# Optimization experiments

Measured on AMD Instinct MI355X. Metric: run time of the kernel, lower is better.

Reference implementation:

```python
import jax, jax.numpy as jnp
import numpy as np

NUM_HEADS = 16
INACTIVE = 4          # cfg_comp.attention_heads_inactive
SIG_DIM = 64          # cfg_comp.attention_heads_signature_dim
MLP_HIDDEN = 512      # cfg_comp.attention_heads_inference_mlp_hidden


def setup_inputs() -> dict:
    key = jax.random.key(0)
    ks = jax.random.split(key, 16)
    S, B, E = 2048, 2, 1024
    def xavier(k, shape, gain=1.0):
        fan_in, fan_out = shape[1], shape[0]
        a = gain * np.sqrt(6.0 / (fan_in + fan_out))
        return jax.random.uniform(k, shape, jnp.float32, -a, a)
    g = 1.0 / np.sqrt(2.0)
    return {
        "query": jax.random.normal(ks[0], (S, B, E), jnp.float32),
        "q_w": xavier(ks[1], (E, E), g), "q_b": jnp.zeros((E,), jnp.float32),
        "k_w": xavier(ks[2], (E, E), g), "k_b": jnp.zeros((E,), jnp.float32),
        "v_w": xavier(ks[3], (E, E), g), "v_b": jnp.zeros((E,), jnp.float32),
        "out_w": xavier(ks[4], (E, E)), "out_b": jnp.zeros((E,), jnp.float32),
        "inf1_w": xavier(ks[5], (MLP_HIDDEN, E), np.sqrt(2.0)),
        "inf1_b": jnp.zeros((MLP_HIDDEN,), jnp.float32),
        "inf2_w": xavier(ks[6], (SIG_DIM, MLP_HIDDEN), np.sqrt(2.0)),
        "inf2_b": jnp.zeros((SIG_DIM,), jnp.float32),
        "head_sig": jax.random.normal(ks[7], (NUM_HEADS, SIG_DIM), jnp.float32)
                    * np.sqrt(2.0 / (NUM_HEADS + SIG_DIM)),
    }


def _head_mask(query, inf1_w, inf1_b, inf2_w, inf2_b, head_sig):
    # inference_masking_step: (S, B, E) -> binary mask (B, H, S)
    t = jax.nn.relu(query @ inf1_w.T + inf1_b)          # (S, B, hidden)
    t = t @ inf2_w.T + inf2_b                            # (S, B, sig)
    s = t @ head_sig.T                                   # (S, B, H) head scores
    keep = NUM_HEADS - INACTIVE
    kth = jax.lax.top_k(s, keep)[0][..., -1]             # (S, B) kth-largest score
    mask = (s >= kth[..., None]).astype(query.dtype)     # 1 at top-`keep` heads
    mask = jax.lax.stop_gradient(mask)                   # scatter of constants in torch
    return jnp.transpose(mask, (1, 2, 0))                # (B, H, S)


def reference(query, q_w, q_b, k_w, k_b, v_w, v_b, out_w, out_b,
              inf1_w, inf1_b, inf2_w, inf2_b, head_sig):
    S, B, E = query.shape
    H, D = NUM_HEADS, E // NUM_HEADS
    scaling = D ** (-0.5)

    q = (query @ q_w.T + q_b) * scaling                  # (S, B, E)
    k = query @ k_w.T + k_b
    v = query @ v_w.T + v_b
    # (S, B, E) -> (B, H, S, D)
    to_bhsd = lambda x: jnp.transpose(x.reshape(S, B, H, D), (1, 2, 0, 3))
    q, k, v = to_bhsd(q), to_bhsd(k), to_bhsd(v)

    attn = jax.nn.softmax(jnp.einsum("bhqd,bhkd->bhqk", q, k), axis=-1)
    o = jnp.einsum("bhqk,bhkd->bhqd", attn, v)           # (B, H, S, D)

    mask = _head_mask(query, inf1_w, inf1_b, inf2_w, inf2_b, head_sig)  # (B, H, S)
    o = o * mask[..., None]                              # gate per head per position

    out = jnp.transpose(o, (2, 0, 1, 3)).reshape(S, B, E)
    return out @ out_w.T + out_b
```

## Files before the change

kernel.cpp:

```cpp
#include <hip/hip_runtime.h>
#include <hip/hip_bf16.h>

#define S_LEN 2048
#define BATCH 2
#define EDIM 1024
#define NHEAD 16
#define DHEAD 64
#define HIDDEN 512
#define SIGD 64
#define KEEP 12

typedef __attribute__((ext_vector_type(8))) short bf16x8;
typedef __attribute__((ext_vector_type(4))) float f32x4;

static __device__ __forceinline__ float bf2f(short s) {
  unsigned int u = ((unsigned int)(unsigned short)s) << 16;
  float f; __builtin_memcpy(&f, &u, 4); return f;
}
static __device__ __forceinline__ short f2bf(float f) {
  unsigned int u; __builtin_memcpy(&u, &f, 4);
  u += 0x7fffu + ((u >> 16) & 1u);
  return (short)(u >> 16);
}

static __device__ __forceinline__ void gl_lds16(const short* g, short* l) {
  __builtin_amdgcn_global_load_lds(
      (const __attribute__((address_space(1))) unsigned int*)g,
      (__attribute__((address_space(3))) unsigned int*)l, 16, 0, 0);
}

template<int CTRL>
static __device__ __forceinline__ float dpp_movf(float x) {
  return __builtin_bit_cast(float, __builtin_amdgcn_update_dpp(
      0, __builtin_bit_cast(int, x), CTRL, 0xF, 0xF, true));
}
static __device__ __forceinline__ float row_max16(float v) {
  v = fmaxf(v, dpp_movf<0x128>(v));
  v = fmaxf(v, dpp_movf<0x124>(v));
  v = fmaxf(v, dpp_movf<0x122>(v));
  v = fmaxf(v, dpp_movf<0x121>(v));
  return v;
}
static __device__ __forceinline__ float row_sum16(float v) {
  v += dpp_movf<0x128>(v);
  v += dpp_movf<0x124>(v);
  v += dpp_movf<0x122>(v);
  v += dpp_movf<0x121>(v);
  return v;
}

__global__ __launch_bounds__(256) void cvt_bf16_kernel(
    const float* __restrict__ in, short* __restrict__ out)
{
  int i = (blockIdx.x * 256 + threadIdx.x) * 4;
  float4 f = *(const float4*)(in + i);
  union { short s[4]; uint2 v; } u;
  u.s[0] = f2bf(f.x); u.s[1] = f2bf(f.y); u.s[2] = f2bf(f.z); u.s[3] = f2bf(f.w);
  *(uint2*)(out + i) = u.v;
}

__global__ __launch_bounds__(256) void cvt3w_kernel(
    const float* __restrict__ qw, const float* __restrict__ kw,
    const float* __restrict__ vw,
    short* __restrict__ Wq, short* __restrict__ Wk, short* __restrict__ Wv)
{
  int blk = blockIdx.x;
  int mat = blk >> 10, sub = blk & 1023;
  const float* in = (mat == 0) ? qw : (mat == 1) ? kw : vw;
  short* out      = (mat == 0) ? Wq : (mat == 1) ? Wk : Wv;
  int i = (sub * 256 + threadIdx.x) * 4;
  float4 f = *(const float4*)(in + i);
  union { short s[4]; uint2 v; } u;
  u.s[0] = f2bf(f.x); u.s[1] = f2bf(f.y); u.s[2] = f2bf(f.z); u.s[3] = f2bf(f.w);
  *(uint2*)(out + i) = u.v;
}

__global__ __launch_bounds__(256) void cvt_split_fused(
    const float* __restrict__ q,  short* __restrict__ qh,  short* __restrict__ ql,
    const float* __restrict__ w1, short* __restrict__ w1h, short* __restrict__ w1l)
{
  int blk = blockIdx.x;
  const float* in; short *oh, *ol; int i;
  if (blk < 4096) { in = q;  oh = qh;  ol = ql;  i = (blk * 256 + threadIdx.x) * 4; }
  else            { in = w1; oh = w1h; ol = w1l; i = ((blk - 4096) * 256 + threadIdx.x) * 4; }
  float4 f = *(const float4*)(in + i);
  union { short s[4]; uint2 v; } uh, ul;
  float x[4] = {f.x, f.y, f.z, f.w};
  #pragma unroll
  for (int u = 0; u < 4; ++u) {
    short h = f2bf(x[u]);
    uh.s[u] = h;
    ul.s[u] = f2bf(x[u] - bf2f(h));
  }
  *(uint2*)(oh + i) = uh.v;
  *(uint2*)(ol + i) = ul.v;
}

template<bool F32OUT>
static __device__ __forceinline__ void gemm128_body(
    const short* __restrict__ A, const short* __restrict__ B,
    const float* __restrict__ bias, void* __restrict__ outv,
    int row0, int col0, float scale)
{
  __shared__ __attribute__((aligned(16))) short As[128*32];
  __shared__ __attribute__((aligned(16))) short Bs[128*32];
  const int tid  = threadIdx.x;
  const int wave = tid >> 6, lane = tid & 63;
  const int quad = lane >> 4, l16 = lane & 15;
  const int wr = wave >> 1, wc = wave & 1;
  const int lr = lane >> 2, lc8 = (lane & 3) * 8;

  const short* gA = A + (size_t)(row0 + wave*16 + lr) * EDIM + lc8;
  const short* gB = B + (size_t)(col0 + wave*16 + lr) * EDIM + lc8;
  short* lA = As + wave*512;
  short* lB = Bs + wave*512;

  f32x4 acc[4][4] = {};
  gl_lds16(gA, lA);  gl_lds16(gA + 64*EDIM, lA + 64*32);
  gl_lds16(gB, lB);  gl_lds16(gB + 64*EDIM, lB + 64*32);

  for (int k0 = 0; k0 < EDIM; k0 += 32) {
    __syncthreads();
    bf16x8 af[4], bfr[4];
    #pragma unroll
    for (int i = 0; i < 4; ++i)
      af[i] = *(const bf16x8*)&As[(wr*64 + i*16 + l16)*32 + quad*8];
    #pragma unroll
    for (int j = 0; j < 4; ++j)
      bfr[j] = *(const bf16x8*)&Bs[(wc*64 + j*16 + l16)*32 + quad*8];
    __syncthreads();
    if (k0 + 32 < EDIM) {
      const short* gA2 = gA + k0 + 32;
      const short* gB2 = gB + k0 + 32;
      gl_lds16(gA2, lA);  gl_lds16(gA2 + 64*EDIM, lA + 64*32);
      gl_lds16(gB2, lB);  gl_lds16(gB2 + 64*EDIM, lB + 64*32);
    }
    #pragma unroll
    for (int i = 0; i < 4; ++i)
      #pragma unroll
      for (int j = 0; j < 4; ++j)
        acc[i][j] = __builtin_amdgcn_mfma_f32_16x16x32_bf16(af[i], bfr[j], acc[i][j], 0, 0, 0);
  }
  #pragma unroll
  for (int j = 0; j < 4; ++j) {
    int col = col0 + wc*64 + j*16 + l16;
    float bv = bias[col];
    #pragma unroll
    for (int i = 0; i < 4; ++i) {
      int rowb = row0 + wr*64 + i*16 + quad*4;
      #pragma unroll
      for (int r = 0; r < 4; ++r) {
        float v = (acc[i][j][r] + bv) * scale;
        if constexpr (F32OUT) {
          ((float*)outv)[(size_t)(rowb + r) * EDIM + col] = v;
        } else {
          ((short*)outv)[(size_t)(rowb + r) * EDIM + col] = f2bf(v);
        }
      }
    }
  }
}

__global__ __launch_bounds__(256) void gemm_qkv(
    const short* __restrict__ A,
    const short* __restrict__ Wq, const short* __restrict__ Wk, const short* __restrict__ Wv,
    const float* __restrict__ qb, const float* __restrict__ kb, const float* __restrict__ vb,
    short* __restrict__ Qp, short* __restrict__ Kp, short* __restrict__ Vp)
{
  int mat = blockIdx.y >> 3, cb = blockIdx.y & 7;
  const short* B   = (mat == 0) ? Wq : (mat == 1) ? Wk : Wv;
  const float* bia = (mat == 0) ? qb : (mat == 1) ? kb : vb;
  short* out       = (mat == 0) ? Qp : (mat == 1) ? Kp : Vp;
  float scale      = (mat == 0) ? 0.125f : 1.0f;
  gemm128_body<false>(A, B, bia, (void*)out, blockIdx.x * 128, cb * 128, scale);
}

__global__ __launch_bounds__(256) void gemm_out(
    const short* __restrict__ A, const short* __restrict__ W,
    const float* __restrict__ bias, float* __restrict__ out)
{
  gemm128_body<true>(A, W, bias, (void*)out, blockIdx.x * 128, blockIdx.y * 128, 1.0f);
}

__global__ __launch_bounds__(256) void gemm_t1_128(
    const short* __restrict__ Agh, const short* __restrict__ Agl,
    const short* __restrict__ Bgh, const short* __restrict__ Bgl,
    const float* __restrict__ bias, float* __restrict__ T1)
{
  __shared__ __attribute__((aligned(16))) short Ah[128*32], Al[128*32];
  __shared__ __attribute__((aligned(16))) short Bh[64*32],  Bl[64*32];
  const int tid  = threadIdx.x;
  const int wave = tid >> 6, lane = tid & 63;
  const int quad = lane >> 4, l16 = lane & 15;
  const int wr = wave >> 1, wc = wave & 1;
  const int lr = lane >> 2, lc8 = (lane & 3) * 8;
  const int row0 = blockIdx.x * 128, col0 = blockIdx.y * 64;

  const short* gAh = Agh + (size_t)(row0 + wave*16 + lr) * EDIM + lc8;
  const short* gAl = Agl + (size_t)(row0 + wave*16 + lr) * EDIM + lc8;
  const short* gBh = Bgh + (size_t)(col0 + wave*16 + lr) * EDIM + lc8;
  const short* gBl = Bgl + (size_t)(col0 + wave*16 + lr) * EDIM + lc8;
  short* lAh = Ah + wave*512;  short* lAl = Al + wave*512;
  short* lBh = Bh + wave*512;  short* lBl = Bl + wave*512;

  f32x4 acc[4][2] = {};
  gl_lds16(gAh, lAh);  gl_lds16(gAh + 64*EDIM, lAh + 64*32);
  gl_lds16(gAl, lAl);  gl_lds16(gAl + 64*EDIM, lAl + 64*32);
  gl_lds16(gBh, lBh);  gl_lds16(gBl, lBl);

  for (int k0 = 0; k0 < EDIM; k0 += 32) {
    __syncthreads();
    bf16x8 ah[4], al[4], bh[2], bl[2];
    #pragma unroll
    for (int i = 0; i < 4; ++i) {
      ah[i] = *(const bf16x8*)&Ah[(wr*64 + i*16 + l16)*32 + quad*8];
      al[i] = *(const bf16x8*)&Al[(wr*64 + i*16 + l16)*32 + quad*8];
    }
    #pragma unroll
    for (int j = 0; j < 2; ++j) {
      bh[j] = *(const bf16x8*)&Bh[(wc*32 + j*16 + l16)*32 + quad*8];
      bl[j] = *(const bf16x8*)&Bl[(wc*32 + j*16 + l16)*32 + quad*8];
    }
    __syncthreads();
    if (k0 + 32 < EDIM) {
      const short* p;
      p = gAh + k0 + 32;  gl_lds16(p, lAh);  gl_lds16(p + 64*EDIM, lAh + 64*32);
      p = gAl + k0 + 32;  gl_lds16(p, lAl);  gl_lds16(p + 64*EDIM, lAl + 64*32);
      gl_lds16(gBh + k0 + 32, lBh);  gl_lds16(gBl + k0 + 32, lBl);
    }
    #pragma unroll
    for (int i = 0; i < 4; ++i)
      #pragma unroll
      for (int j = 0; j < 2; ++j) {
        acc[i][j] = __builtin_amdgcn_mfma_f32_16x16x32_bf16(ah[i], bh[j], acc[i][j], 0, 0, 0);
        acc[i][j] = __builtin_amdgcn_mfma_f32_16x16x32_bf16(ah[i], bl[j], acc[i][j], 0, 0, 0);
        acc[i][j] = __builtin_amdgcn_mfma_f32_16x16x32_bf16(al[i], bh[j], acc[i][j], 0, 0, 0);
      }
  }
  #pragma unroll
  for (int j = 0; j < 2; ++j) {
    int col = col0 + wc*32 + j*16 + l16;
    float bv = bias[col];
    #pragma unroll
    for (int i = 0; i < 4; ++i) {
      int rowb = row0 + wr*64 + i*16 + quad*4;
      #pragma unroll
      for (int r = 0; r < 4; ++r)
        T1[(size_t)(rowb + r) * HIDDEN + col] = fmaxf(acc[i][j][r] + bv, 0.0f);
    }
  }
}

__global__ __launch_bounds__(256) void head_mask16(
    const float* __restrict__ T1, const float* __restrict__ inf2_w,
    const float* __restrict__ inf2_b, const float* __restrict__ head_sig,
    float* __restrict__ maskbuf)
{
  __shared__ float t1s[16][HIDDEN];
  __shared__ float t2s[16][SIGD];
  __shared__ float ss[16][NHEAD];
  const int tid = threadIdx.x;
  const int tok0 = blockIdx.x * 16;
  {
    int row = tid >> 4, c0 = (tid & 15) * 32;
    const float* src = T1 + (size_t)(tok0 + row) * HIDDEN + c0;
    #pragma unroll
    for (int u = 0; u < 8; ++u)
      *(float4*)&t1s[row][c0 + u*4] = *(const float4*)(src + u*4);
  }
  __syncthreads();
  #pragma unroll
  for (int it = 0; it < 4; ++it) {
    int idx = tid + it * 256;
    int tok = idx >> 6, j = idx & 63;
    const float4* w4 = (const float4*)(inf2_w + (size_t)j * HIDDEN);
    const float4* t4 = (const float4*)(&t1s[tok][0]);
    float a = inf2_b[j];
    for (int k = 0; k < HIDDEN/4; ++k) {
      float4 wv = w4[k], tv = t4[k];
      a += tv.x*wv.x + tv.y*wv.y + tv.z*wv.z + tv.w*wv.w;
    }
    t2s[tok][j] = a;
  }
  __syncthreads();
  {
    int tok = tid >> 4, h = tid & 15;
    float a = 0.f;
    for (int d = 0; d < SIGD; ++d) a += t2s[tok][d] * head_sig[h*SIGD + d];
    ss[tok][h] = a;
  }
  __syncthreads();
  {
    int tok = tid >> 4, h = tid & 15;
    float sv = ss[tok][h];
    int cnt = 0;
    #pragma unroll
    for (int j = 0; j < NHEAD; ++j) cnt += (ss[tok][j] > sv) ? 1 : 0;
    int gt = tok0 + tok;
    int s = gt >> 1, b = gt & 1;
    maskbuf[((size_t)(b*NHEAD + h)) * S_LEN + s] = (cnt < KEEP) ? 1.0f : 0.0f;
  }
}

__global__ __launch_bounds__(256) void transpose_v(
    const short* __restrict__ Vp, short* __restrict__ VT)
{
  __shared__ short tile[64][72];
  const int s0 = blockIdx.x * 64, e0 = blockIdx.y * 64, b = blockIdx.z;
  const int t = threadIdx.x;
  {
    int sr = t >> 2, ec = (t & 3) * 16;
    const short* src = Vp + (size_t)(s0 + sr) * 2048 + b * 1024 + e0 + ec;
    *(uint4*)&tile[sr][ec]     = *(const uint4*)src;
    *(uint4*)&tile[sr][ec + 8] = *(const uint4*)(src + 8);
  }
  __syncthreads();
  {
    int er = t >> 2, sc = (t & 3) * 16;
    unsigned pack[8];
    #pragma unroll
    for (int u = 0; u < 8; ++u) {
      unsigned lo = (unsigned short)tile[sc + 2*u][er];
      unsigned hi = (unsigned short)tile[sc + 2*u + 1][er];
      pack[u] = lo | (hi << 16);
    }
    short* dst = VT + (size_t)(b * 1024 + e0 + er) * 2048 + s0 + sc;
    *(uint4*)(dst)     = *(uint4*)&pack[0];
    *(uint4*)(dst + 8) = *(uint4*)&pack[4];
  }
}

__global__ __launch_bounds__(256) void flash_attn(
    short* QpOg, const short* __restrict__ Kp, const short* __restrict__ VT,
    const float* __restrict__ maskbuf)
{
  __shared__ __attribute__((aligned(16))) short Ks[128][72];
  __shared__ __attribute__((aligned(16))) short Vt[64*136];
  __shared__ __attribute__((aligned(16))) short uni[8704];
  const int bh = blockIdx.x;
  const int b = bh >> 4, h = bh & 15;
  const int q0 = blockIdx.y * 64;
  const int tid = threadIdx.x;
  const int wave = tid >> 6, lane = tid & 63;
  const int quad = lane >> 4, l16 = lane & 15;
  const size_t colbase = (size_t)b * EDIM + h * DHEAD;
  const size_t rstride = (size_t)BATCH * EDIM;
  const short* VTbase = VT + (size_t)(bh * 64) * S_LEN;
  {
    int r = tid >> 2, d0 = (tid & 3) * 16;
    const short* src = QpOg + (size_t)(q0 + r) * rstride + colbase + d0;
    *(uint4*)&uni[r*72 + d0]     = *(const uint4*)src;
    *(uint4*)&uni[r*72 + d0 + 8] = *(const uint4*)(src + 8);
  }
  __syncthreads();
  bf16x8 aq0 = *(const bf16x8*)&uni[(wave*16 + l16)*72 + quad*8];
  bf16x8 aq1 = *(const bf16x8*)&uni[(wave*16 + l16)*72 + 32 + quad*8];
  short* Psw = &uni[wave * 2176];

  float m_i[4], l_i[4];
  f32x4 oacc[4];
  #pragma unroll
  for (int r = 0; r < 4; ++r) { m_i[r] = -1e30f; l_i[r] = 0.f; }
  #pragma unroll
  for (int dt = 0; dt < 4; ++dt) oacc[dt] = f32x4{0.f, 0.f, 0.f, 0.f};

  const int vd  = tid >> 2;
  const int vcc = (((tid & 3) + vd) & 3) * 32;

  for (int kv0 = 0; kv0 < S_LEN; kv0 += 128) {
    __syncthreads();
    {
      int r = tid >> 1, c0 = (tid & 1) * 32;
      const short* src = Kp + (size_t)(kv0 + r) * rstride + colbase + c0;
      short* dst = &Ks[r][c0];
      *(uint4*)(dst)      = *(const uint4*)(src);
      *(uint4*)(dst + 8)  = *(const uint4*)(src + 8);
      *(uint4*)(dst + 16) = *(const uint4*)(src + 16);
      *(uint4*)(dst + 24) = *(const uint4*)(src + 24);
    }
    {
      const short* src = VTbase + (size_t)vd * S_LEN + kv0 + vcc;
      short* dst = &Vt[vd*136 + vcc];
      *(uint4*)(dst)      = *(const uint4*)(src);
      *(uint4*)(dst + 8)  = *(const uint4*)(src + 8);
      *(uint4*)(dst + 16) = *(const uint4*)(src + 16);
      *(uint4*)(dst + 24) = *(const uint4*)(src + 24);
    }
    __syncthreads();
    f32x4 sacc[8];
    #pragma unroll
    for (int c = 0; c < 8; ++c) sacc[c] = f32x4{0.f, 0.f, 0.f, 0.f};
    #pragma unroll
    for (int c = 0; c < 8; ++c) {
      bf16x8 b0 = *(const bf16x8*)&Ks[c*16 + l16][quad*8];
      bf16x8 b1 = *(const bf16x8*)&Ks[c*16 + l16][32 + quad*8];
      sacc[c] = __builtin_amdgcn_mfma_f32_16x16x32_bf16(aq0, b0, sacc[c], 0, 0, 0);
      sacc[c] = __builtin_amdgcn_mfma_f32_16x16x32_bf16(aq1, b1, sacc[c], 0, 0, 0);
    }
    #pragma unroll
    for (int r = 0; r < 4; ++r) {
      float vmax = sacc[0][r];
      #pragma unroll
      for (int c = 1; c < 8; ++c) vmax = fmaxf(vmax, sacc[c][r]);
      vmax = row_max16(vmax);
      float mnew = fmaxf(m_i[r], vmax);
      float alpha = __expf(m_i[r] - mnew);
      float rsum = 0.f;
      short* prow = &Psw[(quad*4 + r)*136 + l16];
      #pragma unroll
      for (int p = 0; p < 4; ++p) {
        float ea = __expf(sacc[2*p][r]   - mnew);
        float eb = __expf(sacc[2*p+1][r] - mnew);
        unsigned pk = __builtin_amdgcn_perm(
            __builtin_bit_cast(unsigned, eb),
            __builtin_bit_cast(unsigned, ea), 0x07060302u);
        prow[(2*p)*16]     = (short)(pk & 0xffffu);
        prow[(2*p + 1)*16] = (short)(pk >> 16);
        rsum += __builtin_bit_cast(float, pk << 16);
        rsum += __builtin_bit_cast(float, pk & 0xffff0000u);
      }
      rsum = row_sum16(rsum);
      l_i[r] = l_i[r] * alpha + rsum;
      m_i[r] = mnew;
      #pragma unroll
      for (int dt = 0; dt < 4; ++dt) oacc[dt][r] *= alpha;
    }
    asm volatile("s_waitcnt lgkmcnt(0)" ::: "memory");
    #pragma unroll
    for (int ks = 0; ks < 4; ++ks) {
      bf16x8 ap = *(const bf16x8*)&Psw[l16*136 + ks*32 + quad*8];
      #pragma unroll
      for (int dt = 0; dt < 4; ++dt) {
        bf16x8 bb = *(const bf16x8*)&Vt[(dt*16 + l16)*136 + ks*32 + quad*8];
        oacc[dt] = __builtin_amdgcn_mfma_f32_16x16x32_bf16(ap, bb, oacc[dt], 0, 0, 0);
      }
    }
  }
  #pragma unroll
  for (int r = 0; r < 4; ++r) {
    int s = q0 + wave*16 + quad*4 + r;
    float mk = maskbuf[((size_t)(b*NHEAD + h)) * S_LEN + s];
    float scale = mk / l_i[r];
    short* dst = QpOg + (size_t)s * rstride + colbase;
    #pragma unroll
    for (int dt = 0; dt < 4; ++dt)
      dst[dt*16 + l16] = f2bf(oacc[dt][r] * scale);
  }
}

extern "C" void kernel_launch(void* const* d_in, const int* in_sizes, int n_in,
                              void* d_out, int out_size, void* d_ws, size_t ws_size,
                              hipStream_t stream)
{
  const float* query   = (const float*)d_in[0];
  const float* q_w     = (const float*)d_in[1];
  const float* q_b     = (const float*)d_in[2];
  const float* k_w     = (const float*)d_in[3];
  const float* k_b     = (const float*)d_in[4];
  const float* v_w     = (const float*)d_in[5];
  const float* v_b     = (const float*)d_in[6];
  const float* out_w   = (const float*)d_in[7];
  const float* out_b   = (const float*)d_in[8];
  const float* inf1_w  = (const float*)d_in[9];
  const float* inf1_b  = (const float*)d_in[10];
  const float* inf2_w  = (const float*)d_in[11];
  const float* inf2_b  = (const float*)d_in[12];
  const float* head_sig= (const float*)d_in[13];

  char* ws = (char*)d_ws;
  short* qh = (short*)(ws);
  short* VTb= (short*)(ws);
  short* ql = (short*)(ws + (size_t)( 8u<<20));
  short* Qp = (short*)(ws + (size_t)( 8u<<20));
  short* Kp = (short*)(ws + (size_t)(16u<<20));
  short* Vp = (short*)(ws + (size_t)(24u<<20));
  short* Wo = (short*)(ws + (size_t)(24u<<20));
  char* ob = (char*)d_out;
  float* T1      = (float*)(ob);
  short* Wq      = (short*)(ob);
  short* Wk      = (short*)(ob + (size_t)( 2u<<20));
  short* Wv      = (short*)(ob + (size_t)( 4u<<20));
  short* w1h     = (short*)(ob + (size_t)( 8u<<20));
  short* w1l     = (short*)(ob + (size_t)( 9u<<20));
  float* maskbuf = (float*)(ob + (size_t)(10u<<20));
  float* out     = (float*)d_out;

  dim3 blk(256);
  cvt_split_fused<<<dim3(4608), blk, 0, stream>>>(query, qh, ql, inf1_w, w1h, w1l);
  gemm_t1_128<<<dim3(32, 8), blk, 0, stream>>>(qh, ql, w1h, w1l, inf1_b, T1);
  head_mask16<<<dim3(256), blk, 0, stream>>>(T1, inf2_w, inf2_b, head_sig, maskbuf);
  cvt3w_kernel<<<dim3(3072), blk, 0, stream>>>(q_w, k_w, v_w, Wq, Wk, Wv);
  gemm_qkv<<<dim3(32, 24), blk, 0, stream>>>(qh, Wq, Wk, Wv, q_b, k_b, v_b, Qp, Kp, Vp);
  transpose_v<<<dim3(32, 16, 2), blk, 0, stream>>>(Vp, VTb);
  flash_attn<<<dim3(32, 32), blk, 0, stream>>>(Qp, Kp, VTb, maskbuf);
  cvt_bf16_kernel<<<dim3(1024), blk, 0, stream>>>(out_w, Wo);
  gemm_out<<<dim3(32, 8), blk, 0, stream>>>(Qp, Wo, out_b, out);
}
```

Baseline: 369.3 us.

## Split-K the mask MLP GEMM three ways and use exp2 softmax with prescaled Q

The first mask-MLP GEMM (token x hidden) is split along K into three slices launched as a 3-deep grid. Each slice writes an fp32 partial into spare workspace, and the head-mask kernel sums the partials and applies ReLU. This raises the block count from 256 to 768 so more CUs stay busy. Separately, Q is prescaled by log2(e)/8 so the flash attention softmax can use the native exp2 instruction. The row sum now accumulates the fp32 exponentials instead of the bf16-rounded ones, which slightly changes numerics and adds extra partial-buffer traffic.

```diff
diff --git a/kernel.cpp b/kernel.cpp
--- a/kernel.cpp
+++ b/kernel.cpp
@@ -22,6 +22,12 @@
   u += 0x7fffu + ((u >> 16) & 1u);
   return (short)(u >> 16);
 }
+
+#if __has_builtin(__builtin_amdgcn_exp2f)
+static __device__ __forceinline__ float fexp2(float x) { return __builtin_amdgcn_exp2f(x); }
+#else
+static __device__ __forceinline__ float fexp2(float x) { return exp2f(x); }
+#endif
 
 static __device__ __forceinline__ void gl_lds16(const short* g, short* l) {
   __builtin_amdgcn_global_load_lds(
@@ -171,7 +177,7 @@
   const short* B   = (mat == 0) ? Wq : (mat == 1) ? Wk : Wv;
   const float* bia = (mat == 0) ? qb : (mat == 1) ? kb : vb;
   short* out       = (mat == 0) ? Qp : (mat == 1) ? Kp : Vp;
-  float scale      = (mat == 0) ? 0.125f : 1.0f;
+  float scale      = (mat == 0) ? 0.18033688011112042f : 1.0f;
   gemm128_body<false>(A, B, bia, (void*)out, blockIdx.x * 128, cb * 128, scale);
 }
 
@@ -185,7 +191,8 @@
 __global__ __launch_bounds__(256) void gemm_t1_128(
     const short* __restrict__ Agh, const short* __restrict__ Agl,
     const short* __restrict__ Bgh, const short* __restrict__ Bgl,
-    const float* __restrict__ bias, float* __restrict__ T1)
+    const float* __restrict__ bias,
+    float* __restrict__ P0, float* __restrict__ P1, float* __restrict__ P2)
 {
   __shared__ __attribute__((aligned(16))) short Ah[128*32], Al[128*32];
   __shared__ __attribute__((aligned(16))) short Bh[64*32],  Bl[64*32];
@@ -195,6 +202,9 @@
   const int wr = wave >> 1, wc = wave & 1;
   const int lr = lane >> 2, lc8 = (lane & 3) * 8;
   const int row0 = blockIdx.x * 128, col0 = blockIdx.y * 64;
+  const int z = blockIdx.z;
+  const int kb = z * 352, ke = (z < 2) ? kb + 352 : EDIM;
+  float* P = (z == 0) ? P0 : (z == 1) ? P1 : P2;
 
   const short* gAh = Agh + (size_t)(row0 + wave*16 + lr) * EDIM + lc8;
   const short* gAl = Agl + (size_t)(row0 + wave*16 + lr) * EDIM + lc8;
@@ -204,11 +214,11 @@
   short* lBh = Bh + wave*512;  short* lBl = Bl + wave*512;
 
   f32x4 acc[4][2] = {};
-  gl_lds16(gAh, lAh);  gl_lds16(gAh + 64*EDIM, lAh + 64*32);
-  gl_lds16(gAl, lAl);  gl_lds16(gAl + 64*EDIM, lAl + 64*32);
-  gl_lds16(gBh, lBh);  gl_lds16(gBl, lBl);
-
-  for (int k0 = 0; k0 < EDIM; k0 += 32) {
+  gl_lds16(gAh + kb, lAh);  gl_lds16(gAh + kb + 64*EDIM, lAh + 64*32);
+  gl_lds16(gAl + kb, lAl);  gl_lds16(gAl + kb + 64*EDIM, lAl + 64*32);
+  gl_lds16(gBh + kb, lBh);  gl_lds16(gBl + kb, lBl);
+
+  for (int k0 = kb; k0 < ke; k0 += 32) {
     __syncthreads();
     bf16x8 ah[4], al[4], bh[2], bl[2];
     #pragma unroll
@@ -222,7 +232,7 @@
       bl[j] = *(const bf16x8*)&Bl[(wc*32 + j*16 + l16)*32 + quad*8];
     }
     __syncthreads();
-    if (k0 + 32 < EDIM) {
+    if (k0 + 32 < ke) {
       const short* p;
       p = gAh + k0 + 32;  gl_lds16(p, lAh);  gl_lds16(p + 64*EDIM, lAh + 64*32);
       p = gAl + k0 + 32;  gl_lds16(p, lAl);  gl_lds16(p + 64*EDIM, lAl + 64*32);
@@ -240,19 +250,20 @@
   #pragma unroll
   for (int j = 0; j < 2; ++j) {
     int col = col0 + wc*32 + j*16 + l16;
-    float bv = bias[col];
+    float bv = (z == 0) ? bias[col] : 0.0f;
     #pragma unroll
     for (int i = 0; i < 4; ++i) {
       int rowb = row0 + wr*64 + i*16 + quad*4;
       #pragma unroll
       for (int r = 0; r < 4; ++r)
-        T1[(size_t)(rowb + r) * HIDDEN + col] = fmaxf(acc[i][j][r] + bv, 0.0f);
+        P[(size_t)(rowb + r) * HIDDEN + col] = acc[i][j][r] + bv;
     }
   }
 }
 
 __global__ __launch_bounds__(256) void head_mask16(
-    const float* __restrict__ T1, const float* __restrict__ inf2_w,
+    const float* __restrict__ P0, const float* __restrict__ P1,
+    const float* __restrict__ P2, const float* __restrict__ inf2_w,
     const float* __restrict__ inf2_b, const float* __restrict__ head_sig,
     float* __restrict__ maskbuf)
 {
@@ -263,10 +274,19 @@
   const int tok0 = blockIdx.x * 16;
   {
     int row = tid >> 4, c0 = (tid & 15) * 32;
-    const float* src = T1 + (size_t)(tok0 + row) * HIDDEN + c0;
-    #pragma unroll
-    for (int u = 0; u < 8; ++u)
-      *(float4*)&t1s[row][c0 + u*4] = *(const float4*)(src + u*4);
+    size_t base = (size_t)(tok0 + row) * HIDDEN + c0;
+    #pragma unroll
+    for (int u = 0; u < 8; ++u) {
+      float4 a = *(const float4*)(P0 + base + u*4);
+      float4 b = *(const float4*)(P1 + base + u*4);
+      float4 c = *(const float4*)(P2 + base + u*4);
+      float4 r;
+      r.x = fmaxf(a.x + b.x + c.x, 0.0f);
+      r.y = fmaxf(a.y + b.y + c.y, 0.0f);
+      r.z = fmaxf(a.z + b.z + c.z, 0.0f);
+      r.w = fmaxf(a.w + b.w + c.w, 0.0f);
+      *(float4*)&t1s[row][c0 + u*4] = r;
+    }
   }
   __syncthreads();
   #pragma unroll
@@ -404,20 +424,19 @@
       for (int c = 1; c < 8; ++c) vmax = fmaxf(vmax, sacc[c][r]);
       vmax = row_max16(vmax);
       float mnew = fmaxf(m_i[r], vmax);
-      float alpha = __expf(m_i[r] - mnew);
+      float alpha = fexp2(m_i[r] - mnew);
       float rsum = 0.f;
       short* prow = &Psw[(quad*4 + r)*136 + l16];
       #pragma unroll
       for (int p = 0; p < 4; ++p) {
-        float ea = __expf(sacc[2*p][r]   - mnew);
-        float eb = __expf(sacc[2*p+1][r] - mnew);
+        float ea = fexp2(sacc[2*p][r]   - mnew);
+        float eb = fexp2(sacc[2*p+1][r] - mnew);
         unsigned pk = __builtin_amdgcn_perm(
             __builtin_bit_cast(unsigned, eb),
             __builtin_bit_cast(unsigned, ea), 0x07060302u);
         prow[(2*p)*16]     = (short)(pk & 0xffffu);
         prow[(2*p + 1)*16] = (short)(pk >> 16);
-        rsum += __builtin_bit_cast(float, pk << 16);
-        rsum += __builtin_bit_cast(float, pk & 0xffff0000u);
+        rsum += ea + eb;
       }
       rsum = row_sum16(rsum);
       l_i[r] = l_i[r] * alpha + rsum;
@@ -472,11 +491,13 @@
   short* VTb= (short*)(ws);
   short* ql = (short*)(ws + (size_t)( 8u<<20));
   short* Qp = (short*)(ws + (size_t)( 8u<<20));
+  float* T1p1 = (float*)(ws + (size_t)(16u<<20));
   short* Kp = (short*)(ws + (size_t)(16u<<20));
+  float* T1p2 = (float*)(ws + (size_t)(24u<<20));
   short* Vp = (short*)(ws + (size_t)(24u<<20));
   short* Wo = (short*)(ws + (size_t)(24u<<20));
   char* ob = (char*)d_out;
-  float* T1      = (float*)(ob);
+  float* T1p0    = (float*)(ob);
   short* Wq      = (short*)(ob);
   short* Wk      = (short*)(ob + (size_t)( 2u<<20));
   short* Wv      = (short*)(ob + (size_t)( 4u<<20));
@@ -487,8 +508,10 @@
 
   dim3 blk(256);
   cvt_split_fused<<<dim3(4608), blk, 0, stream>>>(query, qh, ql, inf1_w, w1h, w1l);
-  gemm_t1_128<<<dim3(32, 8), blk, 0, stream>>>(qh, ql, w1h, w1l, inf1_b, T1);
-  head_mask16<<<dim3(256), blk, 0, stream>>>(T1, inf2_w, inf2_b, head_sig, maskbuf);
+  gemm_t1_128<<<dim3(32, 8, 3), blk, 0, stream>>>(qh, ql, w1h, w1l, inf1_b,
+                                                  T1p0, T1p1, T1p2);
+  head_mask16<<<dim3(256), blk, 0, stream>>>(T1p0, T1p1, T1p2,
+                                             inf2_w, inf2_b, head_sig, maskbuf);
   cvt3w_kernel<<<dim3(3072), blk, 0, stream>>>(q_w, k_w, v_w, Wq, Wk, Wv);
   gemm_qkv<<<dim3(32, 24), blk, 0, stream>>>(qh, Wq, Wk, Wv, q_b, k_b, v_b, Qp, Kp, Vp);
   transpose_v<<<dim3(32, 16, 2), blk, 0, stream>>>(Vp, VTb);
```

After: 349.9 us. 5.3% less time.

## Merge conversion, GEMM, and mask/transpose launches into fewer fused kernels

Applied to the files above, without the earlier changes.

All fp32-to-bf16 conversions go into one launch. The T1 and QKV GEMMs are interleaved in a single grid so they run together, and the head-mask and V-transpose kernels are merged into one launch, taking the launch count from nine to five. Softmax now uses exp2, with log2(e) folded into the Q scale, and sums the fp32 exponentials instead of their bf16-rounded values. The workspace layout is changed to fit the new overlap. This trades launch gaps and tail idle time for larger, heterogeneous grids, with a small numerical change in the softmax normalization.

```diff
diff --git a/kernel.cpp b/kernel.cpp
--- a/kernel.cpp
+++ b/kernel.cpp
@@ -23,6 +23,12 @@
   return (short)(u >> 16);
 }
 
+#if __has_builtin(__builtin_amdgcn_exp2f)
+static __device__ __forceinline__ float fexp2(float x) { return __builtin_amdgcn_exp2f(x); }
+#else
+static __device__ __forceinline__ float fexp2(float x) { return exp2f(x); }
+#endif
+
 static __device__ __forceinline__ void gl_lds16(const short* g, short* l) {
   __builtin_amdgcn_global_load_lds(
       (const __attribute__((address_space(1))) unsigned int*)g,
@@ -49,61 +55,53 @@
   return v;
 }
 
-__global__ __launch_bounds__(256) void cvt_bf16_kernel(
-    const float* __restrict__ in, short* __restrict__ out)
-{
-  int i = (blockIdx.x * 256 + threadIdx.x) * 4;
-  float4 f = *(const float4*)(in + i);
-  union { short s[4]; uint2 v; } u;
-  u.s[0] = f2bf(f.x); u.s[1] = f2bf(f.y); u.s[2] = f2bf(f.z); u.s[3] = f2bf(f.w);
-  *(uint2*)(out + i) = u.v;
-}
-
-__global__ __launch_bounds__(256) void cvt3w_kernel(
+__global__ __launch_bounds__(256) void cvt_all(
+    const float* __restrict__ query, const float* __restrict__ inf1_w,
     const float* __restrict__ qw, const float* __restrict__ kw,
-    const float* __restrict__ vw,
-    short* __restrict__ Wq, short* __restrict__ Wk, short* __restrict__ Wv)
+    const float* __restrict__ vw, const float* __restrict__ ow,
+    short* __restrict__ qh, short* __restrict__ ql,
+    short* __restrict__ w1h, short* __restrict__ w1l,
+    short* __restrict__ Wq, short* __restrict__ Wk,
+    short* __restrict__ Wv, short* __restrict__ Wo)
 {
   int blk = blockIdx.x;
-  int mat = blk >> 10, sub = blk & 1023;
-  const float* in = (mat == 0) ? qw : (mat == 1) ? kw : vw;
-  short* out      = (mat == 0) ? Wq : (mat == 1) ? Wk : Wv;
-  int i = (sub * 256 + threadIdx.x) * 4;
-  float4 f = *(const float4*)(in + i);
-  union { short s[4]; uint2 v; } u;
-  u.s[0] = f2bf(f.x); u.s[1] = f2bf(f.y); u.s[2] = f2bf(f.z); u.s[3] = f2bf(f.w);
-  *(uint2*)(out + i) = u.v;
-}
-
-__global__ __launch_bounds__(256) void cvt_split_fused(
-    const float* __restrict__ q,  short* __restrict__ qh,  short* __restrict__ ql,
-    const float* __restrict__ w1, short* __restrict__ w1h, short* __restrict__ w1l)
-{
-  int blk = blockIdx.x;
-  const float* in; short *oh, *ol; int i;
-  if (blk < 4096) { in = q;  oh = qh;  ol = ql;  i = (blk * 256 + threadIdx.x) * 4; }
-  else            { in = w1; oh = w1h; ol = w1l; i = ((blk - 4096) * 256 + threadIdx.x) * 4; }
-  float4 f = *(const float4*)(in + i);
-  union { short s[4]; uint2 v; } uh, ul;
-  float x[4] = {f.x, f.y, f.z, f.w};
-  #pragma unroll
-  for (int u = 0; u < 4; ++u) {
-    short h = f2bf(x[u]);
-    uh.s[u] = h;
-    ul.s[u] = f2bf(x[u] - bf2f(h));
-  }
-  *(uint2*)(oh + i) = uh.v;
-  *(uint2*)(ol + i) = ul.v;
+  if (blk < 4608) {
+    const float* in; short *oh, *ol; int i;
+    if (blk < 4096) { in = query;  oh = qh;  ol = ql;  i = (blk * 256 + threadIdx.x) * 4; }
+    else            { in = inf1_w; oh = w1h; ol = w1l; i = ((blk - 4096) * 256 + threadIdx.x) * 4; }
+    float4 f = *(const float4*)(in + i);
+    union { short s[4]; uint2 v; } uh, ul;
+    float x[4] = {f.x, f.y, f.z, f.w};
+    #pragma unroll
+    for (int u = 0; u < 4; ++u) {
+      short h = f2bf(x[u]);
+      uh.s[u] = h;
+      ul.s[u] = f2bf(x[u] - bf2f(h));
+    }
+    *(uint2*)(oh + i) = uh.v;
+    *(uint2*)(ol + i) = ul.v;
+  } else {
+    int t = blk - 4608;
+    int mat = t >> 10, sub = t & 1023;
+    const float* in = (mat == 0) ? qw : (mat == 1) ? kw : (mat == 2) ? vw : ow;
+    short* out      = (mat == 0) ? Wq : (mat == 1) ? Wk : (mat == 2) ? Wv : Wo;
+    int i = (sub * 256 + threadIdx.x) * 4;
+    float4 f = *(const float4*)(in + i);
+    union { short s[4]; uint2 v; } u;
+    u.s[0] = f2bf(f.x); u.s[1] = f2bf(f.y); u.s[2] = f2bf(f.z); u.s[3] = f2bf(f.w);
+    *(uint2*)(out + i) = u.v;
+  }
 }
 
 template<bool F32OUT>
 static __device__ __forceinline__ void gemm128_body(
+    short* smem,
     const short* __restrict__ A, const short* __restrict__ B,
     const float* __restrict__ bias, void* __restrict__ outv,
     int row0, int col0, float scale)
 {
-  __shared__ __attribute__((aligned(16))) short As[128*32];
-  __shared__ __attribute__((aligned(16))) short Bs[128*32];
+  short* As = smem;
+  short* Bs = smem + 128*32;
   const int tid  = threadIdx.x;
   const int wave = tid >> 6, lane = tid & 63;
   const int quad = lane >> 4, l16 = lane & 15;
@@ -161,40 +159,22 @@
   }
 }
 
-__global__ __launch_bounds__(256) void gemm_qkv(
-    const short* __restrict__ A,
-    const short* __restrict__ Wq, const short* __restrict__ Wk, const short* __restrict__ Wv,
-    const float* __restrict__ qb, const float* __restrict__ kb, const float* __restrict__ vb,
-    short* __restrict__ Qp, short* __restrict__ Kp, short* __restrict__ Vp)
-{
-  int mat = blockIdx.y >> 3, cb = blockIdx.y & 7;
-  const short* B   = (mat == 0) ? Wq : (mat == 1) ? Wk : Wv;
-  const float* bia = (mat == 0) ? qb : (mat == 1) ? kb : vb;
-  short* out       = (mat == 0) ? Qp : (mat == 1) ? Kp : Vp;
-  float scale      = (mat == 0) ? 0.125f : 1.0f;
-  gemm128_body<false>(A, B, bia, (void*)out, blockIdx.x * 128, cb * 128, scale);
-}
-
-__global__ __launch_bounds__(256) void gemm_out(
-    const short* __restrict__ A, const short* __restrict__ W,
-    const float* __restrict__ bias, float* __restrict__ out)
-{
-  gemm128_body<true>(A, W, bias, (void*)out, blockIdx.x * 128, blockIdx.y * 128, 1.0f);
-}
-
-__global__ __launch_bounds__(256) void gemm_t1_128(
+static __device__ __forceinline__ void gemm_t1_body(
+    short* smem,
     const short* __restrict__ Agh, const short* __restrict__ Agl,
     const short* __restrict__ Bgh, const short* __restrict__ Bgl,
-    const float* __restrict__ bias, float* __restrict__ T1)
-{
-  __shared__ __attribute__((aligned(16))) short Ah[128*32], Al[128*32];
-  __shared__ __attribute__((aligned(16))) short Bh[64*32],  Bl[64*32];
+    const float* __restrict__ bias, float* __restrict__ T1,
+    int row0, int col0)
+{
+  short* Ah = smem;
+  short* Al = smem + 4096;
+  short* Bh = smem + 8192;
+  short* Bl = smem + 10240;
   const int tid  = threadIdx.x;
   const int wave = tid >> 6, lane = tid & 63;
   const int quad = lane >> 4, l16 = lane & 15;
   const int wr = wave >> 1, wc = wave & 1;
   const int lr = lane >> 2, lc8 = (lane & 3) * 8;
-  const int row0 = blockIdx.x * 128, col0 = blockIdx.y * 64;
 
   const short* gAh = Agh + (size_t)(row0 + wave*16 + lr) * EDIM + lc8;
   const short* gAl = Agl + (size_t)(row0 + wave*16 + lr) * EDIM + lc8;
@@ -251,82 +231,112 @@
   }
 }
 
-__global__ __launch_bounds__(256) void head_mask16(
+__global__ __launch_bounds__(256) void mega_gemm1(
+    const short* __restrict__ qh, const short* __restrict__ ql,
+    const short* __restrict__ w1h, const short* __restrict__ w1l,
+    const float* __restrict__ inf1_b, float* __restrict__ T1,
+    const short* __restrict__ Wq, const short* __restrict__ Wk,
+    const short* __restrict__ Wv,
+    const float* __restrict__ qb, const float* __restrict__ kb,
+    const float* __restrict__ vb,
+    short* __restrict__ Qp, short* __restrict__ Kp, short* __restrict__ Vp)
+{
+  __shared__ __attribute__((aligned(16))) short smem[12288];
+  int blk = blockIdx.x;
+  if ((blk & 3) == 3) {
+    int id = blk >> 2;
+    gemm_t1_body(smem, qh, ql, w1h, w1l, inf1_b, T1,
+                 (id & 31) * 128, (id >> 5) * 64);
+  } else {
+    int id = (blk >> 2) * 3 + (blk & 3);
+    int row0 = (id & 31) * 128;
+    int rest = id >> 5;
+    int mat = rest >> 3, cb = rest & 7;
+    const short* B   = (mat == 0) ? Wq : (mat == 1) ? Wk : Wv;
+    const float* bia = (mat == 0) ? qb : (mat == 1) ? kb : vb;
+    short* out       = (mat == 0) ? Qp : (mat == 1) ? Kp : Vp;
+    float scale      = (mat == 0) ? 0.18033688011112042f : 1.0f;
+    gemm128_body<false>(smem, qh, B, bia, (void*)out, row0, cb * 128, scale);
+  }
+}
+
+__global__ __launch_bounds__(256) void mid_kernel(
     const float* __restrict__ T1, const float* __restrict__ inf2_w,
     const float* __restrict__ inf2_b, const float* __restrict__ head_sig,
-    float* __restrict__ maskbuf)
-{
-  __shared__ float t1s[16][HIDDEN];
-  __shared__ float t2s[16][SIGD];
-  __shared__ float ss[16][NHEAD];
+    float* __restrict__ maskbuf,
+    const short* __restrict__ Vp, short* __restrict__ VT)
+{
+  __shared__ __attribute__((aligned(16))) float fsm[16*HIDDEN + 16*SIGD + 16*NHEAD];
+  int blk = blockIdx.x;
   const int tid = threadIdx.x;
-  const int tok0 = blockIdx.x * 16;
-  {
-    int row = tid >> 4, c0 = (tid & 15) * 32;
-    const float* src = T1 + (size_t)(tok0 + row) * HIDDEN + c0;
-    #pragma unroll
-    for (int u = 0; u < 8; ++u)
-      *(float4*)&t1s[row][c0 + u*4] = *(const float4*)(src + u*4);
-  }
-  __syncthreads();
-  #pragma unroll
-  for (int it = 0; it < 4; ++it) {
-    int idx = tid + it * 256;
-    int tok = idx >> 6, j = idx & 63;
-    const float4* w4 = (const float4*)(inf2_w + (size_t)j * HIDDEN);
-    const float4* t4 = (const float4*)(&t1s[tok][0]);
-    float a = inf2_b[j];
-    for (int k = 0; k < HIDDEN/4; ++k) {
-      float4 wv = w4[k], tv = t4[k];
-      a += tv.x*wv.x + tv.y*wv.y + tv.z*wv.z + tv.w*wv.w;
-    }
-    t2s[tok][j] = a;
-  }
-  __syncthreads();
-  {
-    int tok = tid >> 4, h = tid & 15;
-    float a = 0.f;
-    for (int d = 0; d < SIGD; ++d) a += t2s[tok][d] * head_sig[h*SIGD + d];
-    ss[tok][h] = a;
-  }
-  __syncthreads();
-  {
-    int tok = tid >> 4, h = tid & 15;
-    float sv = ss[tok][h];
-    int cnt = 0;
-    #pragma unroll
-    for (int j = 0; j < NHEAD; ++j) cnt += (ss[tok][j] > sv) ? 1 : 0;
-    int gt = tok0 + tok;
-    int s = gt >> 1, b = gt & 1;
-    maskbuf[((size_t)(b*NHEAD + h)) * S_LEN + s] = (cnt < KEEP) ? 1.0f : 0.0f;
-  }
-}
-
-__global__ __launch_bounds__(256) void transpose_v(
-    const short* __restrict__ Vp, short* __restrict__ VT)
-{
-  __shared__ short tile[64][72];
-  const int s0 = blockIdx.x * 64, e0 = blockIdx.y * 64, b = blockIdx.z;
-  const int t = threadIdx.x;
-  {
-    int sr = t >> 2, ec = (t & 3) * 16;
-    const short* src = Vp + (size_t)(s0 + sr) * 2048 + b * 1024 + e0 + ec;
-    *(uint4*)&tile[sr][ec]     = *(const uint4*)src;
-    *(uint4*)&tile[sr][ec + 8] = *(const uint4*)(src + 8);
-  }
-  __syncthreads();
-  {
-    int er = t >> 2, sc = (t & 3) * 16;
-    unsigned pack[8];
-    #pragma unroll
-    for (int u = 0; u < 8; ++u) {
-      unsigned lo = (unsigned short)tile[sc + 2*u][er];
-      unsigned hi = (unsigned short)tile[sc + 2*u + 1][er];
-      pack[u] = lo | (hi << 16);
-    }
-    short* dst = VT + (size_t)(b * 1024 + e0 + er) * 2048 + s0 + sc;
-    *(uint4*)(dst)     = *(uint4*)&pack[0];
-    *(uint4*)(dst + 8) = *(uint4*)&pack[4];
+  if (blk < 256) {
+    float (*t1s)[HIDDEN] = (float(*)[HIDDEN])fsm;
+    float (*t2s)[SIGD]   = (float(*)[SIGD])(fsm + 16*HIDDEN);
+    float (*ss)[NHEAD]   = (float(*)[NHEAD])(fsm + 16*HIDDEN + 16*SIGD);
+    const int tok0 = blk * 16;
+    {
+      int row = tid >> 4, c0 = (tid & 15) * 32;
+      const float* src = T1 + (size_t)(tok0 + row) * HIDDEN + c0;
+      #pragma unroll
+      for (int u = 0; u < 8; ++u)
+        *(float4*)&t1s[row][c0 + u*4] = *(const float4*)(src + u*4);
+    }
+    __syncthreads();
+    #pragma unroll
+    for (int it = 0; it < 4; ++it) {
+      int idx = tid + it * 256;
+      int tok = idx >> 6, j = idx & 63;
+      const float4* w4 = (const float4*)(inf2_w + (size_t)j * HIDDEN);
+      const float4* t4 = (const float4*)(&t1s[tok][0]);
+      float a = inf2_b[j];
+      for (int k = 0; k < HIDDEN/4; ++k) {
+        float4 wv = w4[k], tv = t4[k];
+        a += tv.x*wv.x + tv.y*wv.y + tv.z*wv.z + tv.w*wv.w;
+      }
+      t2s[tok][j] = a;
+    }
+    __syncthreads();
+    {
+      int tok = tid >> 4, h = tid & 15;
+      float a = 0.f;
+      for (int d = 0; d < SIGD; ++d) a += t2s[tok][d] * head_sig[h*SIGD + d];
+      ss[tok][h] = a;
+    }
+    __syncthreads();
+    {
+      int tok = tid >> 4, h = tid & 15;
+      float sv = ss[tok][h];
+      int cnt = 0;
+      #pragma unroll
+      for (int j = 0; j < NHEAD; ++j) cnt += (ss[tok][j] > sv) ? 1 : 0;
+      int gt = tok0 + tok;
+      int s = gt >> 1, b = gt & 1;
+      maskbuf[((size_t)(b*NHEAD + h)) * S_LEN + s] = (cnt < KEEP) ? 1.0f : 0.0f;
+    }
+  } else {
+    short (*tile)[72] = (short(*)[72])fsm;
+    int t = blk - 256;
+    const int s0 = (t & 31) * 64, e0 = ((t >> 5) & 15) * 64, b = t >> 9;
+    {
+      int sr = tid >> 2, ec = (tid & 3) * 16;
+      const short* src = Vp + (size_t)(s0 + sr) * 2048 + b * 1024 + e0 + ec;
+      *(uint4*)&tile[sr][ec]     = *(const uint4*)src;
+      *(uint4*)&tile[sr][ec + 8] = *(const uint4*)(src + 8);
+    }
+    __syncthreads();
+    {
+      int er = tid >> 2, sc = (tid & 3) * 16;
+      unsigned pack[8];
+      #pragma unroll
+      for (int u = 0; u < 8; ++u) {
+        unsigned lo = (unsigned short)tile[sc + 2*u][er];
+        unsigned hi = (unsigned short)tile[sc + 2*u + 1][er];
+        pack[u] = lo | (hi << 16);
+      }
+      short* dst = VT + (size_t)(b * 1024 + e0 + er) * 2048 + s0 + sc;
+      *(uint4*)(dst)     = *(uint4*)&pack[0];
+      *(uint4*)(dst + 8) = *(uint4*)&pack[4];
+    }
   }
 }
 
@@ -404,20 +414,19 @@
       for (int c = 1; c < 8; ++c) vmax = fmaxf(vmax, sacc[c][r]);
       vmax = row_max16(vmax);
       float mnew = fmaxf(m_i[r], vmax);
-      float alpha = __expf(m_i[r] - mnew);
+      float alpha = fexp2(m_i[r] - mnew);
       float rsum = 0.f;
       short* prow = &Psw[(quad*4 + r)*136 + l16];
       #pragma unroll
       for (int p = 0; p < 4; ++p) {
-        float ea = __expf(sacc[2*p][r]   - mnew);
-        float eb = __expf(sacc[2*p+1][r] - mnew);
+        float ea = fexp2(sacc[2*p][r]   - mnew);
+        float eb = fexp2(sacc[2*p+1][r] - mnew);
         unsigned pk = __builtin_amdgcn_perm(
             __builtin_bit_cast(unsigned, eb),
             __builtin_bit_cast(unsigned, ea), 0x07060302u);
         prow[(2*p)*16]     = (short)(pk & 0xffffu);
         prow[(2*p + 1)*16] = (short)(pk >> 16);
-        rsum += __builtin_bit_cast(float, pk << 16);
-        rsum += __builtin_bit_cast(float, pk & 0xffff0000u);
+        rsum += ea + eb;
       }
       rsum = row_sum16(rsum);
       l_i[r] = l_i[r] * alpha + rsum;
@@ -446,6 +455,15 @@
     for (int dt = 0; dt < 4; ++dt)
       dst[dt*16 + l16] = f2bf(oacc[dt][r] * scale);
   }
+}
+
+__global__ __launch_bounds__(256) void gemm_out(
+    const short* __restrict__ A, const short* __restrict__ W,
+    const float* __restrict__ bias, float* __restrict__ out)
+{
+  __shared__ __attribute__((aligned(16))) short smem[8192];
+  gemm128_body<true>(smem, A, W, bias, (void*)out,
+                     blockIdx.x * 128, blockIdx.y * 128, 1.0f);
 }
 
 extern "C" void kernel_launch(void* const* d_in, const int* in_sizes, int n_in,
@@ -468,31 +486,30 @@
   const float* head_sig= (const float*)d_in[13];
 
   char* ws = (char*)d_ws;
-  short* qh = (short*)(ws);
-  short* VTb= (short*)(ws);
-  short* ql = (short*)(ws + (size_t)( 8u<<20));
-  short* Qp = (short*)(ws + (size_t)( 8u<<20));
-  short* Kp = (short*)(ws + (size_t)(16u<<20));
-  short* Vp = (short*)(ws + (size_t)(24u<<20));
-  short* Wo = (short*)(ws + (size_t)(24u<<20));
+  short* qh      = (short*)(ws);
+  short* VTb     = (short*)(ws);
+  short* ql      = (short*)(ws + (size_t)( 8u<<20));
+  float* maskbuf = (float*)(ws + (size_t)( 8u<<20));
+  short* Qp      = (short*)(ws + (size_t)(16u<<20));
+  short* Kp      = (short*)(ws + (size_t)(24u<<20));
+  short* Vp      = (short*)(ws + (size_t)(32u<<20));
+  short* Wo      = (short*)(ws + (size_t)(40u<<20));
   char* ob = (char*)d_out;
-  float* T1      = (float*)(ob);
-  short* Wq      = (short*)(ob);
-  short* Wk      = (short*)(ob + (size_t)( 2u<<20));
-  short* Wv      = (short*)(ob + (size_t)( 4u<<20));
-  short* w1h     = (short*)(ob + (size_t)( 8u<<20));
-  short* w1l     = (short*)(ob + (size_t)( 9u<<20));
-  float* maskbuf = (float*)(ob + (size_t)(10u<<20));
-  float* out     = (float*)d_out;
+  float* T1  = (float*)(ob);
+  short* w1h = (short*)(ob + (size_t)( 8u<<20));
+  short* w1l = (short*)(ob + (size_t)( 9u<<20));
+  short* Wq  = (short*)(ob + (size_t)(10u<<20));
+  short* Wk  = (short*)(ob + (size_t)(12u<<20));
+  short* Wv  = (short*)(ob + (size_t)(14u<<20));
+  float* out = (float*)d_out;
 
   dim3 blk(256);
-  cvt_split_fused<<<dim3(4608), blk, 0, stream>>>(query, qh, ql, inf1_w, w1h, w1l);
-  gemm_t1_128<<<dim3(32, 8), blk, 0, stream>>>(qh, ql, w1h, w1l, inf1_b, T1);
-  head_mask16<<<dim3(256), blk, 0, stream>>>(T1, inf2_w, inf2_b, head_sig, maskbuf);
-  cvt3w_kernel<<<dim3(3072), blk, 0, stream>>>(q_w, k_w, v_w, Wq, Wk, Wv);
-  gemm_qkv<<<dim3(32, 24), blk, 0, stream>>>(qh, Wq, Wk, Wv, q_b, k_b, v_b, Qp, Kp, Vp);
-  transpose_v<<<dim3(32, 16, 2), blk, 0, stream>>>(Vp, VTb);
+  cvt_all<<<dim3(8704), blk, 0, stream>>>(query, inf1_w, q_w, k_w, v_w, out_w,
+                                          qh, ql, w1h, w1l, Wq, Wk, Wv, Wo);
+  mega_gemm1<<<dim3(1024), blk, 0, stream>>>(qh, ql, w1h, w1l, inf1_b, T1,
+                                             Wq, Wk, Wv, q_b, k_b, v_b, Qp, Kp, Vp);
+  mid_kernel<<<dim3(1280), blk, 0, stream>>>(T1, inf2_w, inf2_b, head_sig, maskbuf,
+                                             Vp, VTb);
   flash_attn<<<dim3(32, 32), blk, 0, stream>>>(Qp, Kp, VTb, maskbuf);
-  cvt_bf16_kernel<<<dim3(1024), blk, 0, stream>>>(out_w, Wo);
   gemm_out<<<dim3(32, 8), blk, 0, stream>>>(Qp, Wo, out_b, out);
 }
```

After: 337.4 us. 1.09x faster.
